# Performance work log

Hardware: AMD Instinct MI355X
Metric: run time of the kernel (lower is better)

Reference implementation:

```python
import jax, jax.numpy as jnp
import numpy as np
from jax import lax

EPS = 1e-5
CARD = 32


def _bn(x, gamma, beta):
    # training-mode BatchNorm2d: batch statistics over (N, H, W) per channel
    mean = jnp.mean(x, axis=(0, 2, 3), keepdims=True)
    var = jnp.var(x, axis=(0, 2, 3), keepdims=True)
    inv = lax.rsqrt(var + EPS)
    return gamma[None, :, None, None] * (x - mean) * inv + beta[None, :, None, None]


def _conv(x, w, stride=1, padding='VALID', groups=1):
    return lax.conv_general_dilated(
        x, w, window_strides=(stride, stride), padding=padding,
        dimension_numbers=('NCHW', 'OIHW', 'NCHW'),
        feature_group_count=groups)


def setup_inputs() -> dict:
    key = jax.random.key(0)
    ks = jax.random.split(key, 4)
    N, Cin, H, W = 32, 256, 56, 56
    D, Cout = 16, 256
    CD = CARD * D  # 512
    x = jax.random.normal(ks[0], (N, Cin, H, W), dtype=jnp.float32)
    w1 = jax.random.normal(ks[1], (CD, Cin, 1, 1), dtype=jnp.float32) * 0.05
    w3 = jax.random.normal(ks[2], (CD, D, 3, 3), dtype=jnp.float32) * 0.05
    wa = jax.random.normal(ks[3], (Cout, CD, 1, 1), dtype=jnp.float32) * 0.05
    return {
        'x': x,
        'w1': w1, 'g1': jnp.ones(CD), 'b1': jnp.zeros(CD),
        'w3': w3, 'g3': jnp.ones(CD), 'b3': jnp.zeros(CD),
        'wa': wa, 'ga': jnp.ones(Cout), 'ba': jnp.zeros(Cout),
    }


def reference(x, w1, g1, b1, w3, g3, b3, wa, ga, ba):
    # 32 paths of (1x1 conv -> BN -> ReLU -> 3x3 conv -> BN -> ReLU) then concat
    # is exactly: one 1x1 conv to 512ch -> BN -> ReLU -> grouped 3x3 conv (32 groups)
    # -> BN -> ReLU  (per-channel BN commutes with channel concatenation).
    out = _conv(x, w1)                                   # [N, 512, H, W]
    out = jax.nn.relu(_bn(out, g1, b1))
    out = _conv(out, w3, stride=1, padding=((1, 1), (1, 1)), groups=CARD)
    out = jax.nn.relu(_bn(out, g3, b3))
    out = _conv(out, wa)                                 # [N, 256, H, W]
    out = _bn(out, ga, ba)
    out = out + x                                        # identity shortcut (stride=1, Cin==Cout)
    return jax.nn.relu(out)
```

## Files before the change

### kernel.cpp

```cpp
#include <hip/hip_runtime.h>

#define HW 3136
#define NPOS 100352.0f
#define NSLICE 32

typedef unsigned short ushortT;
typedef __attribute__((ext_vector_type(8))) short short8;
typedef __attribute__((ext_vector_type(4))) float floatx4;

__device__ inline float bf2f(ushortT u) {
    union { unsigned int i; float f; } v; v.i = ((unsigned int)u) << 16; return v.f;
}
__device__ inline ushortT f2bf(float f) {
    union { float f; unsigned int i; } v; v.f = f;
    unsigned int r = v.i + 0x7FFFu + ((v.i >> 16) & 1u);
    return (ushortT)(r >> 16);
}

__global__ __launch_bounds__(256) void prep_k(const float* __restrict__ w1,
                                              const float* __restrict__ w3,
                                              const float* __restrict__ wa,
                                              ushortT* __restrict__ w1b,
                                              ushortT* __restrict__ wab,
                                              ushortT* __restrict__ w3b,
                                              float* __restrict__ partials) {
    int i = blockIdx.x * 256 + threadIdx.x;
    if (i < 131072) { w1b[i] = f2bf(w1[i]); wab[i] = f2bf(wa[i]); }
    if (i < 81920) {
        int ic = i & 15, oc = (i >> 4) & 15, rest = i >> 8;
        int s = rest % 10, g = rest / 10;
        w3b[i] = (s < 9) ? f2bf(w3[(((g * 16 + oc) * 16) + ic) * 9 + s]) : (ushortT)0;
        partials[i] = 0.f;
    }
}

__global__ __launch_bounds__(256) void transx_k(const float* __restrict__ x,
                                                ushortT* __restrict__ xb) {
    __shared__ float tf[64 * 65];
    const int t = threadIdx.x;
    const int p0 = blockIdx.x * 64, k0 = blockIdx.y * 64, n = blockIdx.z;
#pragma unroll
    for (int i = 0; i < 16; i++) {
        int idx = t + i * 256;
        int k = idx >> 6, p = idx & 63;
        tf[k * 65 + p] = x[((size_t)n * 256 + k0 + k) * HW + p0 + p];
    }
    __syncthreads();
#pragma unroll
    for (int i = 0; i < 2; i++) {
        int idx = t + i * 256;
        int p = idx >> 3, kq = (idx & 7) * 8;
        short8 o;
#pragma unroll
        for (int j = 0; j < 8; j++) o[j] = (short)f2bf(tf[(kq + j) * 65 + p]);
        *(short8*)&xb[((size_t)n * HW + p0 + p) * 256 + k0 + kq] = o;
    }
}

__global__ __launch_bounds__(256) void gemm1_k(const ushortT* __restrict__ xb,
                                               const ushortT* __restrict__ w1b,
                                               ushortT* __restrict__ t1,
                                               float* __restrict__ p1) {
    __shared__ ushortT As[128 * 40];
    __shared__ ushortT Bs[128 * 40];
    const int t = threadIdx.x;
    const int P0 = blockIdx.x * 128, C0 = blockIdx.y * 128, n = blockIdx.z;
    const int w = t >> 6, lane = t & 63;
    const int mh = (w >> 1) * 64, nh = (w & 1) * 64;
    const int l15 = lane & 15, quad = lane >> 4;
    const int sr = t >> 2, skq = (t & 3) * 8;

    floatx4 acc[4][4];
#pragma unroll
    for (int a = 0; a < 4; a++)
#pragma unroll
        for (int b = 0; b < 4; b++)
#pragma unroll
            for (int e = 0; e < 4; e++) acc[a][b][e] = 0.f;

    for (int kb = 0; kb < 256; kb += 32) {
#pragma unroll
        for (int i = 0; i < 2; i++) {
            int r = sr + i * 64;
            short8 v = *(const short8*)&w1b[(size_t)(C0 + r) * 256 + kb + skq];
            *(short8*)&As[r * 40 + skq] = v;
        }
#pragma unroll
        for (int i = 0; i < 2; i++) {
            int p = sr + i * 64;
            short8 v;
            if (P0 + p < HW) {
                v = *(const short8*)&xb[((size_t)n * HW + P0 + p) * 256 + kb + skq];
            } else {
#pragma unroll
                for (int j = 0; j < 8; j++) v[j] = 0;
            }
            *(short8*)&Bs[p * 40 + skq] = v;
        }
        __syncthreads();
        short8 af[4], bf[4];
#pragma unroll
        for (int mt = 0; mt < 4; mt++)
            af[mt] = *(const short8*)&As[(mh + mt * 16 + l15) * 40 + quad * 8];
#pragma unroll
        for (int nt = 0; nt < 4; nt++)
            bf[nt] = *(const short8*)&Bs[(nh + nt * 16 + l15) * 40 + quad * 8];
#pragma unroll
        for (int mt = 0; mt < 4; mt++)
#pragma unroll
            for (int nt = 0; nt < 4; nt++)
                acc[mt][nt] = __builtin_amdgcn_mfma_f32_16x16x32_bf16(af[mt], bf[nt], acc[mt][nt], 0, 0, 0);
        __syncthreads();
    }
#pragma unroll
    for (int mt = 0; mt < 4; mt++) {
        int c = C0 + mh + mt * 16 + quad * 4;
#pragma unroll
        for (int nt = 0; nt < 4; nt++) {
            int pp = P0 + nh + nt * 16 + l15;
            if (pp < HW) {
                ushort4 o;
                o.x = f2bf(acc[mt][nt][0]); o.y = f2bf(acc[mt][nt][1]);
                o.z = f2bf(acc[mt][nt][2]); o.w = f2bf(acc[mt][nt][3]);
                *(ushort4*)&t1[((size_t)n * HW + pp) * 512 + c] = o;
            }
        }
    }
    float* ps = p1 + ((blockIdx.x + blockIdx.z * 25) & (NSLICE - 1)) * 1024;
#pragma unroll
    for (int mt = 0; mt < 4; mt++) {
        int c = C0 + mh + mt * 16 + quad * 4;
#pragma unroll
        for (int e = 0; e < 4; e++) {
            float sv = acc[mt][0][e] + acc[mt][1][e] + acc[mt][2][e] + acc[mt][3][e];
            float qv = acc[mt][0][e] * acc[mt][0][e] + acc[mt][1][e] * acc[mt][1][e]
                     + acc[mt][2][e] * acc[mt][2][e] + acc[mt][3][e] * acc[mt][3][e];
            sv += __shfl_xor(sv, 1); qv += __shfl_xor(qv, 1);
            sv += __shfl_xor(sv, 2); qv += __shfl_xor(qv, 2);
            sv += __shfl_xor(sv, 4); qv += __shfl_xor(qv, 4);
            sv += __shfl_xor(sv, 8); qv += __shfl_xor(qv, 8);
            if (l15 == 0) {
                atomicAdd(&ps[c + e], sv);
                atomicAdd(&ps[512 + c + e], qv);
            }
        }
    }
}

__global__ __launch_bounds__(256) void gconv_k(const ushortT* __restrict__ t1,
                                               const ushortT* __restrict__ w3b,
                                               const float* __restrict__ p1,
                                               const float* __restrict__ g1,
                                               const float* __restrict__ b1,
                                               ushortT* __restrict__ t2,
                                               float* __restrict__ p2) {
    __shared__ ushortT tile[8 * 590 * 8];
    __shared__ float scs[64], shs[64];
    const int t = threadIdx.x;
    const int rt = blockIdx.x, gg = blockIdx.y, n = blockIdx.z;
    const int r0 = rt * 8;

    if (t < 64) {
        int c = gg * 64 + t;
        float S = 0.f, Q = 0.f;
#pragma unroll
        for (int s = 0; s < NSLICE; s++) {
            S += p1[s * 1024 + c];
            Q += p1[s * 1024 + 512 + c];
        }
        float m = S * (1.f / NPOS);
        float var = Q * (1.f / NPOS) - m * m;
        float sc = g1[c] * rsqrtf(var + 1e-5f);
        scs[t] = sc; shs[t] = b1[c] - m * sc;
    }
    __syncthreads();

    const int chq = t & 7;
    float sc8[8], sh8[8];
#pragma unroll
    for (int j = 0; j < 8; j++) { sc8[j] = scs[chq * 8 + j]; sh8[j] = shs[chq * 8 + j]; }

    const ushortT* src = t1 + (size_t)n * HW * 512 + gg * 64 + chq * 8;
    for (int idx = t; idx < 4640; idx += 256) {
        int pos = idx >> 3;
        int row = pos / 58, col = pos - row * 58;
        int ir = r0 - 1 + row, icl = col - 1;
        short8 o;
        if (ir >= 0 && ir < 56 && icl >= 0 && icl < 56) {
            short8 v = *(const short8*)&src[(size_t)(ir * 56 + icl) * 512];
#pragma unroll
            for (int j = 0; j < 8; j++)
                o[j] = (short)f2bf(fmaxf(fmaf(sc8[j], bf2f((ushortT)v[j]), sh8[j]), 0.f));
        } else {
#pragma unroll
            for (int j = 0; j < 8; j++) o[j] = 0;
        }
        *(short8*)&tile[((chq * 590) + row * 59 + col) * 8] = o;
    }
    __syncthreads();

    const int w = t >> 6, lane = t & 63;
    const int l15 = lane & 15, quad = lane >> 4;
    const int qh = quad >> 1, ql = quad & 1;
    const int g = gg * 4 + w;

    short8 af[5];
    int drv[5], dcv[5];
#pragma unroll
    for (int s = 0; s < 5; s++) {
        int shift = 2 * s + qh;
        af[s] = *(const short8*)&w3b[((g * 10 + shift) * 16 + l15) * 16 + ql * 8];
        if (shift == 9) shift = 8;
        drv[s] = shift / 3; dcv[s] = shift - drv[s] * 3;
    }

    const int pr = l15 >> 2, pc = l15 & 3;
    const int plane = (w * 2 + ql) * 590;
    float s4[4] = {0.f, 0.f, 0.f, 0.f}, q4[4] = {0.f, 0.f, 0.f, 0.f};

#pragma unroll
    for (int rh = 0; rh < 2; rh++) {
        const int rbase = rh * 4 + pr;
        floatx4 acc[14];
#pragma unroll
        for (int ct = 0; ct < 14; ct++)
#pragma unroll
            for (int e = 0; e < 4; e++) acc[ct][e] = 0.f;

#pragma unroll
        for (int ct = 0; ct < 14; ct++) {
            int colb = ct * 4 + pc;
#pragma unroll
            for (int s = 0; s < 5; s++) {
                short8 bfv = *(const short8*)&tile[(plane + (rbase + drv[s]) * 59 + colb + dcv[s]) * 8];
                acc[ct] = __builtin_amdgcn_mfma_f32_16x16x32_bf16(af[s], bfv, acc[ct], 0, 0, 0);
            }
        }
#pragma unroll
        for (int ct = 0; ct < 14; ct++) {
            int pos = (r0 + rh * 4 + pr) * 56 + ct * 4 + pc;
            ushort4 o;
            o.x = f2bf(acc[ct][0]); o.y = f2bf(acc[ct][1]);
            o.z = f2bf(acc[ct][2]); o.w = f2bf(acc[ct][3]);
            *(ushort4*)&t2[((size_t)n * HW + pos) * 512 + g * 16 + quad * 4] = o;
#pragma unroll
            for (int e = 0; e < 4; e++) {
                float a = acc[ct][e];
                s4[e] += a; q4[e] += a * a;
            }
        }
    }
    float* ps = p2 + ((blockIdx.x + blockIdx.z * 7) & (NSLICE - 1)) * 1024;
#pragma unroll
    for (int e = 0; e < 4; e++) {
        float sv = s4[e], qv = q4[e];
        sv += __shfl_xor(sv, 1); qv += __shfl_xor(qv, 1);
        sv += __shfl_xor(sv, 2); qv += __shfl_xor(qv, 2);
        sv += __shfl_xor(sv, 4); qv += __shfl_xor(qv, 4);
        sv += __shfl_xor(sv, 8); qv += __shfl_xor(qv, 8);
        if (l15 == 0) {
            atomicAdd(&ps[g * 16 + quad * 4 + e], sv);
            atomicAdd(&ps[512 + g * 16 + quad * 4 + e], qv);
        }
    }
}

__global__ __launch_bounds__(256) void gemm3_k(const ushortT* __restrict__ t2,
                                               const ushortT* __restrict__ wab,
                                               const float* __restrict__ p2,
                                               const float* __restrict__ g3,
                                               const float* __restrict__ b3,
                                               ushortT* __restrict__ t3,
                                               float* __restrict__ p3) {
    __shared__ ushortT As[256 * 40];
    __shared__ ushortT Bs[64 * 40];
    __shared__ float2 scsh[512];
    const int t = threadIdx.x;
    const int P0 = blockIdx.x * 64, n = blockIdx.y;
    const int w = t >> 6, lane = t & 63;
    const int mh = w * 64;
    const int l15 = lane & 15, quad = lane >> 4;
    const int sr = t >> 2, skq = (t & 3) * 8;

#pragma unroll
    for (int i = 0; i < 2; i++) {
        int c = t + i * 256;
        float S = 0.f, Q = 0.f;
#pragma unroll
        for (int s = 0; s < NSLICE; s++) {
            S += p2[s * 1024 + c];
            Q += p2[s * 1024 + 512 + c];
        }
        float m = S * (1.f / NPOS);
        float var = Q * (1.f / NPOS) - m * m;
        float sc = g3[c] * rsqrtf(var + 1e-5f);
        scsh[c] = make_float2(sc, b3[c] - m * sc);
    }
    __syncthreads();

    floatx4 acc[4][4];
#pragma unroll
    for (int a = 0; a < 4; a++)
#pragma unroll
        for (int b = 0; b < 4; b++)
#pragma unroll
            for (int e = 0; e < 4; e++) acc[a][b][e] = 0.f;

    for (int kb = 0; kb < 512; kb += 32) {
#pragma unroll
        for (int i = 0; i < 4; i++) {
            int r = sr + i * 64;
            short8 v = *(const short8*)&wab[(size_t)r * 512 + kb + skq];
            *(short8*)&As[r * 40 + skq] = v;
        }
        {
            int p = sr;
            short8 v = *(const short8*)&t2[((size_t)n * HW + P0 + p) * 512 + kb + skq];
            short8 o;
#pragma unroll
            for (int j = 0; j < 8; j++) {
                float2 ss = scsh[kb + skq + j];
                o[j] = (short)f2bf(fmaxf(fmaf(ss.x, bf2f((ushortT)v[j]), ss.y), 0.f));
            }
            *(short8*)&Bs[p * 40 + skq] = o;
        }
        __syncthreads();
        short8 af[4], bf[4];
#pragma unroll
        for (int mt = 0; mt < 4; mt++)
            af[mt] = *(const short8*)&As[(mh + mt * 16 + l15) * 40 + quad * 8];
#pragma unroll
        for (int nt = 0; nt < 4; nt++)
            bf[nt] = *(const short8*)&Bs[(nt * 16 + l15) * 40 + quad * 8];
#pragma unroll
        for (int mt = 0; mt < 4; mt++)
#pragma unroll
            for (int nt = 0; nt < 4; nt++)
                acc[mt][nt] = __builtin_amdgcn_mfma_f32_16x16x32_bf16(af[mt], bf[nt], acc[mt][nt], 0, 0, 0);
        __syncthreads();
    }
#pragma unroll
    for (int mt = 0; mt < 4; mt++) {
        int c = mh + mt * 16 + quad * 4;
#pragma unroll
        for (int nt = 0; nt < 4; nt++) {
            int pp = P0 + nt * 16 + l15;
            ushort4 o;
            o.x = f2bf(acc[mt][nt][0]); o.y = f2bf(acc[mt][nt][1]);
            o.z = f2bf(acc[mt][nt][2]); o.w = f2bf(acc[mt][nt][3]);
            *(ushort4*)&t3[((size_t)n * HW + pp) * 256 + c] = o;
        }
    }
    float* ps = p3 + ((blockIdx.x + blockIdx.y * 49) & (NSLICE - 1)) * 512;
#pragma unroll
    for (int mt = 0; mt < 4; mt++) {
        int c = mh + mt * 16 + quad * 4;
#pragma unroll
        for (int e = 0; e < 4; e++) {
            float sv = acc[mt][0][e] + acc[mt][1][e] + acc[mt][2][e] + acc[mt][3][e];
            float qv = acc[mt][0][e] * acc[mt][0][e] + acc[mt][1][e] * acc[mt][1][e]
                     + acc[mt][2][e] * acc[mt][2][e] + acc[mt][3][e] * acc[mt][3][e];
            sv += __shfl_xor(sv, 1); qv += __shfl_xor(qv, 1);
            sv += __shfl_xor(sv, 2); qv += __shfl_xor(qv, 2);
            sv += __shfl_xor(sv, 4); qv += __shfl_xor(qv, 4);
            sv += __shfl_xor(sv, 8); qv += __shfl_xor(qv, 8);
            if (l15 == 0) {
                atomicAdd(&ps[c + e], sv);
                atomicAdd(&ps[256 + c + e], qv);
            }
        }
    }
}

__global__ __launch_bounds__(256) void final_k(const ushortT* __restrict__ t3,
                                               const float* __restrict__ x,
                                               const float* __restrict__ p3,
                                               const float* __restrict__ ga,
                                               const float* __restrict__ ba,
                                               float* __restrict__ out) {
    __shared__ float tf[64 * 65];
    __shared__ float scs[64], shs[64];
    const int t = threadIdx.x;
    const int p0 = blockIdx.x * 64, c0 = blockIdx.y * 64, n = blockIdx.z;
    if (t < 64) {
        int c = c0 + t;
        float S = 0.f, Q = 0.f;
#pragma unroll
        for (int s = 0; s < NSLICE; s++) {
            S += p3[s * 512 + c];
            Q += p3[s * 512 + 256 + c];
        }
        float m = S * (1.f / NPOS);
        float var = Q * (1.f / NPOS) - m * m;
        float sc = ga[c] * rsqrtf(var + 1e-5f);
        scs[t] = sc; shs[t] = ba[c] - m * sc;
    }
    __syncthreads();
#pragma unroll
    for (int i = 0; i < 4; i++) {
        int idx = t + i * 256;
        int p = idx >> 4, cq = (idx & 15) * 4;
        ushort4 v = *(const ushort4*)&t3[((size_t)n * HW + p0 + p) * 256 + c0 + cq];
        tf[(cq + 0) * 65 + p] = fmaf(scs[cq + 0], bf2f(v.x), shs[cq + 0]);
        tf[(cq + 1) * 65 + p] = fmaf(scs[cq + 1], bf2f(v.y), shs[cq + 1]);
        tf[(cq + 2) * 65 + p] = fmaf(scs[cq + 2], bf2f(v.z), shs[cq + 2]);
        tf[(cq + 3) * 65 + p] = fmaf(scs[cq + 3], bf2f(v.w), shs[cq + 3]);
    }
    __syncthreads();
#pragma unroll
    for (int i = 0; i < 4; i++) {
        int idx = t + i * 256;
        int c = idx >> 4, pq = (idx & 15) * 4;
        size_t off = ((size_t)n * 256 + c0 + c) * HW + p0 + pq;
        float4 xv = *(const float4*)&x[off];
        float4 o;
        o.x = fmaxf(tf[c * 65 + pq + 0] + xv.x, 0.f);
        o.y = fmaxf(tf[c * 65 + pq + 1] + xv.y, 0.f);
        o.z = fmaxf(tf[c * 65 + pq + 2] + xv.z, 0.f);
        o.w = fmaxf(tf[c * 65 + pq + 3] + xv.w, 0.f);
        *(float4*)&out[off] = o;
    }
}

extern "C" void kernel_launch(void* const* d_in, const int* in_sizes, int n_in,
                              void* d_out, int out_size, void* d_ws, size_t ws_size,
                              hipStream_t stream) {
    const float* x  = (const float*)d_in[0];
    const float* w1 = (const float*)d_in[1];
    const float* g1 = (const float*)d_in[2];
    const float* b1 = (const float*)d_in[3];
    const float* w3 = (const float*)d_in[4];
    const float* g3 = (const float*)d_in[5];
    const float* b3 = (const float*)d_in[6];
    const float* wa = (const float*)d_in[7];
    const float* ga = (const float*)d_in[8];
    const float* ba = (const float*)d_in[9];
    float* out = (float*)d_out;

    char* ws = (char*)d_ws;
    ushortT* t1 = (ushortT*)ws;
    ushortT* t3 = t1;
    ushortT* xb = (ushortT*)(ws + 102760448);
    ushortT* t2 = (ushortT*)(ws + 102760448);
    ushortT* w1b = (ushortT*)(ws + 205520896);
    ushortT* wab = (ushortT*)(ws + 205783040);
    ushortT* w3b = (ushortT*)(ws + 206045184);
    float* partials = (float*)(ws + 206209024);
    float* pt1 = partials;
    float* pt2 = partials + 32 * 1024;
    float* pt3 = partials + 64 * 1024;

    prep_k<<<512, 256, 0, stream>>>(w1, w3, wa, w1b, wab, w3b, partials);
    transx_k<<<dim3(49, 4, 32), 256, 0, stream>>>(x, xb);
    gemm1_k<<<dim3(25, 4, 32), 256, 0, stream>>>(xb, w1b, t1, pt1);
    gconv_k<<<dim3(7, 8, 32), 256, 0, stream>>>(t1, w3b, pt1, g1, b1, t2, pt2);
    gemm3_k<<<dim3(49, 32), 256, 0, stream>>>(t2, wab, pt2, g3, b3, t3, pt3);
    final_k<<<dim3(49, 4, 32), 256, 0, stream>>>(t3, x, pt3, ga, ba, out);
}
```

Measured before the change: 501.7 us.

## Use direct global-to-LDS loads with XOR swizzle and K=64 tiles in gemm1

The gemm1 kernel now stages A and B tiles with global_load_lds (direct global-to-LDS DMA) rather than loading through registers and storing to shared memory. The K tile doubles from 32 to 64, which halves the number of barrier pairs. An XOR swizzle on the LDS layout replaces the padded stride to avoid bank conflicts. Out-of-range pixel rows read from a zeroed buffer (pt3, which prep_k zeroes). This relies on that buffer holding zeros when gemm1 runs and on the LDS address layout matching what the global_load_lds builtin expects.

```diff
diff --git a/kernel.cpp b/kernel.cpp
--- a/kernel.cpp
+++ b/kernel.cpp
@@ -15,6 +15,12 @@
     union { float f; unsigned int i; } v; v.f = f;
     unsigned int r = v.i + 0x7FFFu + ((v.i >> 16) & 1u);
     return (ushortT)(r >> 16);
+}
+
+__device__ inline void gl_lds16(const ushortT* g, ushortT* l) {
+    __builtin_amdgcn_global_load_lds(
+        (const __attribute__((address_space(1))) unsigned int*)g,
+        (__attribute__((address_space(3))) unsigned int*)l, 16, 0, 0);
 }
 
 __global__ __launch_bounds__(256) void prep_k(const float* __restrict__ w1,
@@ -59,16 +65,33 @@
 
 __global__ __launch_bounds__(256) void gemm1_k(const ushortT* __restrict__ xb,
                                                const ushortT* __restrict__ w1b,
+                                               const float* __restrict__ zpad,
                                                ushortT* __restrict__ t1,
                                                float* __restrict__ p1) {
-    __shared__ ushortT As[128 * 40];
-    __shared__ ushortT Bs[128 * 40];
+    __shared__ ushortT As[128 * 64];
+    __shared__ ushortT Bs[128 * 64];
     const int t = threadIdx.x;
     const int P0 = blockIdx.x * 128, C0 = blockIdx.y * 128, n = blockIdx.z;
     const int w = t >> 6, lane = t & 63;
     const int mh = (w >> 1) * 64, nh = (w & 1) * 64;
     const int l15 = lane & 15, quad = lane >> 4;
-    const int sr = t >> 2, skq = (t & 3) * 8;
+
+    const int srow = w * 32 + (lane >> 3);
+    const int slin = lane & 7;
+
+    const ushortT* agp[4];
+    const ushortT* bgp[4];
+#pragma unroll
+    for (int i = 0; i < 4; i++) {
+        int row = srow + i * 8;
+        int sl = (slin ^ (row & 7)) * 8;
+        agp[i] = w1b + (size_t)(C0 + row) * 256 + sl;
+        int p = P0 + row;
+        bgp[i] = (p < HW) ? xb + ((size_t)n * HW + p) * 256 + sl
+                          : (const ushortT*)zpad;
+    }
+    ushortT* al = As + (w * 32) * 64;
+    ushortT* bl = Bs + (w * 32) * 64;
 
     floatx4 acc[4][4];
 #pragma unroll
@@ -78,38 +101,33 @@
 #pragma unroll
             for (int e = 0; e < 4; e++) acc[a][b][e] = 0.f;
 
-    for (int kb = 0; kb < 256; kb += 32) {
-#pragma unroll
-        for (int i = 0; i < 2; i++) {
-            int r = sr + i * 64;
-            short8 v = *(const short8*)&w1b[(size_t)(C0 + r) * 256 + kb + skq];
-            *(short8*)&As[r * 40 + skq] = v;
-        }
-#pragma unroll
-        for (int i = 0; i < 2; i++) {
-            int p = sr + i * 64;
-            short8 v;
-            if (P0 + p < HW) {
-                v = *(const short8*)&xb[((size_t)n * HW + P0 + p) * 256 + kb + skq];
-            } else {
-#pragma unroll
-                for (int j = 0; j < 8; j++) v[j] = 0;
-            }
-            *(short8*)&Bs[p * 40 + skq] = v;
-        }
+    for (int kb = 0; kb < 256; kb += 64) {
+#pragma unroll
+        for (int i = 0; i < 4; i++) gl_lds16(agp[i] + kb, al + i * 512);
+#pragma unroll
+        for (int i = 0; i < 4; i++) gl_lds16(bgp[i] + kb, bl + i * 512);
         __syncthreads();
-        short8 af[4], bf[4];
-#pragma unroll
-        for (int mt = 0; mt < 4; mt++)
-            af[mt] = *(const short8*)&As[(mh + mt * 16 + l15) * 40 + quad * 8];
-#pragma unroll
-        for (int nt = 0; nt < 4; nt++)
-            bf[nt] = *(const short8*)&Bs[(nh + nt * 16 + l15) * 40 + quad * 8];
-#pragma unroll
-        for (int mt = 0; mt < 4; mt++)
-#pragma unroll
-            for (int nt = 0; nt < 4; nt++)
-                acc[mt][nt] = __builtin_amdgcn_mfma_f32_16x16x32_bf16(af[mt], bf[nt], acc[mt][nt], 0, 0, 0);
+        short8 af[2][4], bfv[2][4];
+#pragma unroll
+        for (int mt = 0; mt < 4; mt++) {
+            int row = mh + mt * 16 + l15, rx = row & 7;
+            af[0][mt] = *(const short8*)&As[row * 64 + ((quad ^ rx) * 8)];
+            af[1][mt] = *(const short8*)&As[row * 64 + (((quad + 4) ^ rx) * 8)];
+        }
+#pragma unroll
+        for (int nt = 0; nt < 4; nt++) {
+            int row = nh + nt * 16 + l15, rx = row & 7;
+            bfv[0][nt] = *(const short8*)&Bs[row * 64 + ((quad ^ rx) * 8)];
+            bfv[1][nt] = *(const short8*)&Bs[row * 64 + (((quad + 4) ^ rx) * 8)];
+        }
+#pragma unroll
+        for (int ks = 0; ks < 2; ks++)
+#pragma unroll
+            for (int mt = 0; mt < 4; mt++)
+#pragma unroll
+                for (int nt = 0; nt < 4; nt++)
+                    acc[mt][nt] = __builtin_amdgcn_mfma_f32_16x16x32_bf16(
+                        af[ks][mt], bfv[ks][nt], acc[mt][nt], 0, 0, 0);
         __syncthreads();
     }
 #pragma unroll
@@ -452,7 +470,7 @@
 
     prep_k<<<512, 256, 0, stream>>>(w1, w3, wa, w1b, wab, w3b, partials);
     transx_k<<<dim3(49, 4, 32), 256, 0, stream>>>(x, xb);
-    gemm1_k<<<dim3(25, 4, 32), 256, 0, stream>>>(xb, w1b, t1, pt1);
+    gemm1_k<<<dim3(25, 4, 32), 256, 0, stream>>>(xb, w1b, pt3, t1, pt1);
     gconv_k<<<dim3(7, 8, 32), 256, 0, stream>>>(t1, w3b, pt1, g1, b1, t2, pt2);
     gemm3_k<<<dim3(49, 32), 256, 0, stream>>>(t2, wab, pt2, g3, b3, t3, pt3);
     final_k<<<dim3(49, 4, 32), 256, 0, stream>>>(t3, x, pt3, ga, ba, out);
```

Result: faster. 468.5 us (-6.6%).
